# Performance work log

Hardware: AMD Instinct MI355X
Metric: run time of the kernel (lower is better)

## Reference

```python
import jax, jax.numpy as jnp
import numpy as np
import math

D, S, B = 64, 2048, 16  # head_dim, seq_len, batch (inputs stored as [D, S, B])


def setup_inputs() -> dict:
    key = jax.random.key(0)
    kq, kk, kv = jax.random.split(key, 3)
    return {
        "Q": jax.random.normal(kq, (D, S, B), dtype=jnp.float32),
        "K": jax.random.normal(kk, (D, S, B), dtype=jnp.float32),
        "V": jax.random.normal(kv, (D, S, B), dtype=jnp.float32),
        "d_k": S,
    }


def reference(Q, K, V, d_k):
    # transpose(0, 2): [D, S, B] -> [B, S, D]
    q = jnp.transpose(Q, (2, 1, 0))
    k = jnp.transpose(K, (2, 1, 0))
    v = jnp.transpose(V, (2, 1, 0))
    # bmm(_Q, K_T) * 1/sqrt(d_k): [B, S, S]
    scores = jnp.einsum("bsd,btd->bst", q, k) * (1.0 / math.sqrt(d_k))
    # original does view(-1, d_k) + Softmax over dim=1; with d_k == last dim
    # this is a softmax over the key axis. Dropout is identity in eval mode.
    probs = jax.nn.softmax(scores, axis=-1)
    out = jnp.einsum("bst,btd->bsd", probs, v)  # [B, S, D]
    # transpose(0, 2) back: [D, S, B]
    return jnp.transpose(out, (2, 1, 0))
```

## Files before the change

kernel.cpp:

```cpp
#include <hip/hip_runtime.h>

#define D_ 64
#define S_ 2048
#define B_ 16
#define QT 64
#define KVT 128

typedef short short8 __attribute__((ext_vector_type(8)));
typedef short short4a __attribute__((ext_vector_type(4)));
typedef float floatx4 __attribute__((ext_vector_type(4)));
typedef unsigned uint2v __attribute__((ext_vector_type(2)));

#define SC2 (1.4426950408889634f / 45.254833995939045f)

__device__ __forceinline__ unsigned short f2bf(float f) {
  unsigned u = __builtin_bit_cast(unsigned, f);
  u += 0x7fffu + ((u >> 16) & 1u);
  return (unsigned short)(u >> 16);
}

__device__ __forceinline__ floatx4 mfma16(short4a a, short4a b, floatx4 c) {
#if __has_builtin(__builtin_amdgcn_mfma_f32_16x16x16bf16_1k)
  return __builtin_amdgcn_mfma_f32_16x16x16bf16_1k(a, b, c, 0, 0, 0);
#else
  floatx4 d;
  asm volatile("v_mfma_f32_16x16x16_bf16 %0, %1, %2, %3"
               : "=v"(d) : "v"(a), "v"(b), "v"(c));
  return d;
#endif
}

__global__ __launch_bounds__(256) void pack_all(const float* __restrict__ Q,
                                                const float* __restrict__ K,
                                                const float* __restrict__ V,
                                                unsigned short* __restrict__ Qp,
                                                unsigned short* __restrict__ Kp,
                                                unsigned short* __restrict__ Vt) {
  __shared__ __align__(16) unsigned short tile[256][72];
  const int t = threadIdx.x;
  const int bid = blockIdx.x;
  if (bid < 256) {
    const bool isK = bid >= 128;
    const float* src = isK ? K : Q;
    unsigned short* dst = isK ? Kp : Qp;
    const float scale = isK ? SC2 : 1.0f;
    const int s0 = (bid & 127) * 16;
#pragma unroll
    for (int i = 0; i < 16; i++) {
      int j = i * 256 + t;
      int d = j >> 6;
      int sb4 = (j & 63) * 4;
      const float4 v = *(const float4*)(src + (size_t)d * (S_ * B_) + s0 * B_ + sb4);
      float vv[4] = {v.x, v.y, v.z, v.w};
#pragma unroll
      for (int k = 0; k < 4; k++) {
        int sb = sb4 + k;
        tile[(sb & 15) * 16 + (sb >> 4)][d] = f2bf(vv[k] * scale);
      }
    }
    __syncthreads();
#pragma unroll
    for (int i = 0; i < 8; i++) {
      int j = i * 256 + t;
      int r = j >> 3, c = j & 7;
      int b = r >> 4, si = r & 15;
      uint4 v = *(const uint4*)(&tile[r][c * 8]);
      *(uint4*)(dst + ((size_t)(b * S_ + s0 + si) * D_ + c * 8)) = v;
    }
  } else {
    const int vb = bid - 256;
    const int s0 = (vb & 31) * 64;
    const int d0 = (vb >> 5) * 16;
#pragma unroll
    for (int i = 0; i < 16; i++) {
      int j = i * 256 + t;
      int dd = j >> 8;
      int sb4 = (j & 255) * 4;
      const float4 v = *(const float4*)(V + (size_t)(d0 + dd) * (S_ * B_) + s0 * B_ + sb4);
      float vv[4] = {v.x, v.y, v.z, v.w};
#pragma unroll
      for (int k = 0; k < 4; k++) {
        int sb = sb4 + k;
        tile[(sb & 15) * 16 + dd][sb >> 4] = f2bf(vv[k]);
      }
    }
    __syncthreads();
#pragma unroll
    for (int i = 0; i < 8; i++) {
      int j = i * 256 + t;
      int r = j >> 3, c = j & 7;
      int b = r >> 4, dd = r & 15;
      uint4 v = *(const uint4*)(&tile[r][c * 8]);
      *(uint4*)(Vt + ((size_t)(b * D_ + d0 + dd) * S_ + s0 + c * 8)) = v;
    }
  }
}

__global__ __launch_bounds__(256, 2) void attn(const unsigned short* __restrict__ Qp,
                                               const unsigned short* __restrict__ Kp,
                                               const unsigned short* __restrict__ Vt,
                                               float* __restrict__ Ot) {
  __shared__ __align__(16) char smem_[69632 + 1024];
  float* red = (float*)smem_;
  float* lred = (float*)(smem_ + 69632);
  unsigned short* Vbuf0 = (unsigned short*)smem_;
  unsigned short* Vbuf1 = (unsigned short*)(smem_ + 17408);

  const int tid = threadIdx.x;
  const int w = tid >> 6, l = tid & 63, g = l >> 4, ln = l & 15;
  const int b = blockIdx.x & 15;
  const int q0 = (int)(blockIdx.x >> 4) * QT;
  const int kvw = w * 32;

  const unsigned short* Qb = Qp + (size_t)b * S_ * D_;
  const unsigned short* Kb = Kp + (size_t)b * S_ * D_;
  const unsigned short* Vb = Vt + (size_t)b * D_ * S_;

  short8 qf[4][2];
#pragma unroll
  for (int nf = 0; nf < 4; nf++)
#pragma unroll
    for (int ks = 0; ks < 2; ks++)
      qf[nf][ks] = *(const short8*)(Qb + (size_t)(q0 + nf * 16 + ln) * D_ + ks * 32 + g * 8);

  short8 kf[2][2];
#pragma unroll
  for (int mf = 0; mf < 2; mf++)
#pragma unroll
    for (int ks = 0; ks < 2; ks++)
      kf[mf][ks] = *(const short8*)(Kb + (size_t)(kvw + mf * 16 + ln) * D_ + ks * 32 + g * 8);

  {
    uint4 vstg[4];
#pragma unroll
    for (int i = 0; i < 4; i++) {
      int idx = i * 256 + tid, r = idx >> 4, c = idx & 15;
      vstg[i] = *(const uint4*)(Vb + (size_t)r * S_ + c * 8);
    }
#pragma unroll
    for (int i = 0; i < 4; i++) {
      int idx = i * 256 + tid, r = idx >> 4, c = idx & 15;
      *(uint4*)(&Vbuf0[r * 136 + c * 8]) = vstg[i];
    }
  }
  __syncthreads();

  const short4a ones = {(short)0x3F80, (short)0x3F80, (short)0x3F80, (short)0x3F80};
  floatx4 oacc[4][4];
  floatx4 dacc[4];
#pragma unroll
  for (int mfd = 0; mfd < 4; mfd++)
#pragma unroll
    for (int nf = 0; nf < 4; nf++) oacc[mfd][nf] = (floatx4){0.f, 0.f, 0.f, 0.f};
#pragma unroll
  for (int nf = 0; nf < 4; nf++) dacc[nf] = (floatx4){0.f, 0.f, 0.f, 0.f};

  for (int t = 0; t < 16; t++) {
    const int kvn = ((t + 1) * KVT) & (S_ - 1);

    uint4 vstg[4];
#pragma unroll
    for (int i = 0; i < 4; i++) {
      int idx = i * 256 + tid, r = idx >> 4, c = idx & 15;
      vstg[i] = *(const uint4*)(Vb + (size_t)r * S_ + kvn + c * 8);
    }

    floatx4 sacc[2][4];
#pragma unroll
    for (int mf = 0; mf < 2; mf++)
#pragma unroll
      for (int nf = 0; nf < 4; nf++) sacc[mf][nf] = (floatx4){0.f, 0.f, 0.f, 0.f};
#pragma unroll
    for (int ks = 0; ks < 2; ks++)
#pragma unroll
      for (int mf = 0; mf < 2; mf++)
#pragma unroll
        for (int nf = 0; nf < 4; nf++)
          sacc[mf][nf] = __builtin_amdgcn_mfma_f32_16x16x32_bf16(kf[mf][ks], qf[nf][ks],
                                                                 sacc[mf][nf], 0, 0, 0);

#pragma unroll
    for (int mf = 0; mf < 2; mf++)
#pragma unroll
      for (int ks = 0; ks < 2; ks++)
        kf[mf][ks] = *(const short8*)(Kb + (size_t)(kvn + kvw + mf * 16 + ln) * D_ + ks * 32 + g * 8);

    short4a pb[2][4];
#pragma unroll
    for (int mf = 0; mf < 2; mf++)
#pragma unroll
      for (int nf = 0; nf < 4; nf++) {
        unsigned u0 = __builtin_bit_cast(unsigned, __builtin_amdgcn_exp2f(sacc[mf][nf][0])) + 0x8000u;
        unsigned u1 = __builtin_bit_cast(unsigned, __builtin_amdgcn_exp2f(sacc[mf][nf][1])) + 0x8000u;
        unsigned u2 = __builtin_bit_cast(unsigned, __builtin_amdgcn_exp2f(sacc[mf][nf][2])) + 0x8000u;
        unsigned u3 = __builtin_bit_cast(unsigned, __builtin_amdgcn_exp2f(sacc[mf][nf][3])) + 0x8000u;
        unsigned lo = __builtin_amdgcn_perm(u1, u0, 0x07060302u);
        unsigned hi = __builtin_amdgcn_perm(u3, u2, 0x07060302u);
        pb[mf][nf] = __builtin_bit_cast(short4a, (uint2v){lo, hi});
      }

#pragma unroll
    for (int mf = 0; mf < 2; mf++)
#pragma unroll
      for (int nf = 0; nf < 4; nf++)
        dacc[nf] = mfma16(ones, pb[mf][nf], dacc[nf]);

    unsigned short* vw = ((t + 1) & 1) ? Vbuf1 : Vbuf0;
#pragma unroll
    for (int i = 0; i < 4; i++) {
      int idx = i * 256 + tid, r = idx >> 4, c = idx & 15;
      *(uint4*)(&vw[r * 136 + c * 8]) = vstg[i];
    }

    const unsigned short* vr = (t & 1) ? Vbuf1 : Vbuf0;
#pragma unroll
    for (int mfd = 0; mfd < 4; mfd++)
#pragma unroll
      for (int mf = 0; mf < 2; mf++) {
        short4a vf = *(const short4a*)(&vr[(mfd * 16 + ln) * 136 + kvw + mf * 16 + g * 4]);
#pragma unroll
        for (int nf = 0; nf < 4; nf++)
          oacc[mfd][nf] = mfma16(vf, pb[mf][nf], oacc[mfd][nf]);
      }
    __syncthreads();
  }

  if (g == 0) {
#pragma unroll
    for (int nf = 0; nf < 4; nf++) lred[w * 64 + nf * 16 + ln] = dacc[nf][0];
  }
#pragma unroll
  for (int mfd = 0; mfd < 4; mfd++)
#pragma unroll
    for (int nf = 0; nf < 4; nf++)
      *(floatx4*)(&red[w * 4352 + (nf * 16 + ln) * 68 + mfd * 16 + g * 4]) = oacc[mfd][nf];
  __syncthreads();

  const int q = l;
  const float denom = lred[q] + lred[64 + q] + lred[128 + q] + lred[192 + q];
  const float linv = 1.0f / denom;
#pragma unroll
  for (int i = 0; i < 4; i++) {
    floatx4 s = (floatx4){0.f, 0.f, 0.f, 0.f};
#pragma unroll
    for (int w2 = 0; w2 < 4; w2++)
      s += *(const floatx4*)(&red[w2 * 4352 + q * 68 + w * 16 + i * 4]);
    s *= linv;
#pragma unroll
    for (int r = 0; r < 4; r++)
      Ot[(size_t)(b * D_ + w * 16 + i * 4 + r) * S_ + q0 + q] = s[r];
  }
}

__global__ __launch_bounds__(256) void unpack_o(const float* __restrict__ Ot,
                                                float* __restrict__ out) {
  const int d0 = (int)(blockIdx.x & 7) * 8;
  const int s0 = (int)(blockIdx.x >> 3) * 64;
  __shared__ float u[8 * 1024];
  const int t = threadIdx.x;
#pragma unroll
  for (int i = 0; i < 8; i++) {
    int j = i * 256 + t;
    int d = j >> 8, bb = (j >> 4) & 15, c = j & 15;
    float4 v = *(const float4*)(Ot + (size_t)(bb * D_ + d0 + d) * S_ + s0 + c * 4);
    float vv[4] = {v.x, v.y, v.z, v.w};
#pragma unroll
    for (int k = 0; k < 4; k++) {
      int si = c * 4 + k;
      int W = si * 16 + bb;
      int Wp = W ^ ((si & 15) << 2);
      u[d * 1024 + Wp] = vv[k];
    }
  }
  __syncthreads();
#pragma unroll
  for (int i = 0; i < 8; i++) {
    int j = i * 256 + t;
    int d = j >> 8, c2 = j & 255;
    int G = c2 ^ ((c2 >> 2) & 15);
    float4 v = *(const float4*)(&u[d * 1024 + G * 4]);
    *(float4*)(out + (size_t)(d0 + d) * (S_ * B_) + s0 * B_ + c2 * 4) = v;
  }
}

extern "C" void kernel_launch(void* const* d_in, const int* in_sizes, int n_in,
                              void* d_out, int out_size, void* d_ws, size_t ws_size,
                              hipStream_t stream) {
  const float* Q = (const float*)d_in[0];
  const float* K = (const float*)d_in[1];
  const float* V = (const float*)d_in[2];
  float* out = (float*)d_out;
  char* ws = (char*)d_ws;
  unsigned short* Qp = (unsigned short*)(ws);
  unsigned short* Kp = (unsigned short*)(ws + (4u << 20));
  unsigned short* Vt = (unsigned short*)(ws + (8u << 20));
  float* Ot = (float*)(ws + (12u << 20));

  hipLaunchKernelGGL(pack_all, dim3(384), dim3(256), 0, stream, Q, K, V, Qp, Kp, Vt);
  hipLaunchKernelGGL(attn, dim3(512), dim3(256), 0, stream, Qp, Kp, Vt, Ot);
  hipLaunchKernelGGL(unpack_o, dim3(256), dim3(256), 0, stream, Ot, out);
}
```

Measured before the change: 110.8 us.

## Load V fragments directly to registers and drop LDS staging and per-tile syncs

The attention loop no longer stages V tiles through double-buffered shared memory with a barrier per tile. Each wave now loads its own V fragments straight from global memory into registers, double-buffered in a manually unrolled two-step loop. The row-sum denominator is accumulated in fp32 with adds and cross-lane shuffles instead of extra MFMAs against a ones vector. The pack kernel's shared tile gets XOR swizzling to cut bank conflicts. In exchange, each wave issues narrow 8-byte strided global loads for V and uses more registers.

```diff
diff --git a/kernel.cpp b/kernel.cpp
--- a/kernel.cpp
+++ b/kernel.cpp
@@ -20,14 +20,7 @@
 }
 
 __device__ __forceinline__ floatx4 mfma16(short4a a, short4a b, floatx4 c) {
-#if __has_builtin(__builtin_amdgcn_mfma_f32_16x16x16bf16_1k)
   return __builtin_amdgcn_mfma_f32_16x16x16bf16_1k(a, b, c, 0, 0, 0);
-#else
-  floatx4 d;
-  asm volatile("v_mfma_f32_16x16x16_bf16 %0, %1, %2, %3"
-               : "=v"(d) : "v"(a), "v"(b), "v"(c));
-  return d;
-#endif
 }
 
 __global__ __launch_bounds__(256) void pack_all(const float* __restrict__ Q,
@@ -55,7 +48,9 @@
 #pragma unroll
       for (int k = 0; k < 4; k++) {
         int sb = sb4 + k;
-        tile[(sb & 15) * 16 + (sb >> 4)][d] = f2bf(vv[k] * scale);
+        int row = (sb & 15) * 16 + (sb >> 4);
+        int sw = (((row >> 3) & 1) << 3) | (((row >> 6) & 3) << 4);
+        tile[row][d ^ sw] = f2bf(vv[k] * scale);
       }
     }
     __syncthreads();
@@ -64,7 +59,8 @@
       int j = i * 256 + t;
       int r = j >> 3, c = j & 7;
       int b = r >> 4, si = r & 15;
-      uint4 v = *(const uint4*)(&tile[r][c * 8]);
+      int sw = (((r >> 3) & 1) << 3) | (((r >> 6) & 3) << 4);
+      uint4 v = *(const uint4*)(&tile[r][(c * 8) ^ sw]);
       *(uint4*)(dst + ((size_t)(b * S_ + s0 + si) * D_ + c * 8)) = v;
     }
   } else {
@@ -81,7 +77,9 @@
 #pragma unroll
       for (int k = 0; k < 4; k++) {
         int sb = sb4 + k;
-        tile[(sb & 15) * 16 + dd][sb >> 4] = f2bf(vv[k]);
+        int row = (sb & 15) * 16 + dd;
+        int sw = ((row >> 6) & 3) << 3;
+        tile[row][(sb >> 4) ^ sw] = f2bf(vv[k]);
       }
     }
     __syncthreads();
@@ -90,7 +88,8 @@
       int j = i * 256 + t;
       int r = j >> 3, c = j & 7;
       int b = r >> 4, dd = r & 15;
-      uint4 v = *(const uint4*)(&tile[r][c * 8]);
+      int sw = ((r >> 6) & 3) << 3;
+      uint4 v = *(const uint4*)(&tile[r][(c * 8) ^ sw]);
       *(uint4*)(Vt + ((size_t)(b * D_ + d0 + dd) * S_ + s0 + c * 8)) = v;
     }
   }
@@ -100,11 +99,8 @@
                                                const unsigned short* __restrict__ Kp,
                                                const unsigned short* __restrict__ Vt,
                                                float* __restrict__ Ot) {
-  __shared__ __align__(16) char smem_[69632 + 1024];
-  float* red = (float*)smem_;
-  float* lred = (float*)(smem_ + 69632);
-  unsigned short* Vbuf0 = (unsigned short*)smem_;
-  unsigned short* Vbuf1 = (unsigned short*)(smem_ + 17408);
+  __shared__ __align__(16) float red[4 * 64 * 68];
+  __shared__ float lred[4 * 64];
 
   const int tid = threadIdx.x;
   const int w = tid >> 6, l = tid & 63, g = l >> 4, ln = l & 15;
@@ -123,47 +119,38 @@
     for (int ks = 0; ks < 2; ks++)
       qf[nf][ks] = *(const short8*)(Qb + (size_t)(q0 + nf * 16 + ln) * D_ + ks * 32 + g * 8);
 
-  short8 kf[2][2];
+  floatx4 oacc[4][4];
+#pragma unroll
+  for (int mfd = 0; mfd < 4; mfd++)
+#pragma unroll
+    for (int nf = 0; nf < 4; nf++) oacc[mfd][nf] = (floatx4){0.f, 0.f, 0.f, 0.f};
+  float lpart[4] = {0.f, 0.f, 0.f, 0.f};
+
+  short8 kfA[2][2], kfB[2][2];
+  short4a vfA[4][2], vfB[4][2];
 #pragma unroll
   for (int mf = 0; mf < 2; mf++)
 #pragma unroll
     for (int ks = 0; ks < 2; ks++)
-      kf[mf][ks] = *(const short8*)(Kb + (size_t)(kvw + mf * 16 + ln) * D_ + ks * 32 + g * 8);
-
-  {
-    uint4 vstg[4];
-#pragma unroll
-    for (int i = 0; i < 4; i++) {
-      int idx = i * 256 + tid, r = idx >> 4, c = idx & 15;
-      vstg[i] = *(const uint4*)(Vb + (size_t)r * S_ + c * 8);
-    }
-#pragma unroll
-    for (int i = 0; i < 4; i++) {
-      int idx = i * 256 + tid, r = idx >> 4, c = idx & 15;
-      *(uint4*)(&Vbuf0[r * 136 + c * 8]) = vstg[i];
-    }
-  }
-  __syncthreads();
-
-  const short4a ones = {(short)0x3F80, (short)0x3F80, (short)0x3F80, (short)0x3F80};
-  floatx4 oacc[4][4];
-  floatx4 dacc[4];
+      kfA[mf][ks] = *(const short8*)(Kb + (size_t)(kvw + mf * 16 + ln) * D_ + ks * 32 + g * 8);
 #pragma unroll
   for (int mfd = 0; mfd < 4; mfd++)
 #pragma unroll
-    for (int nf = 0; nf < 4; nf++) oacc[mfd][nf] = (floatx4){0.f, 0.f, 0.f, 0.f};
-#pragma unroll
-  for (int nf = 0; nf < 4; nf++) dacc[nf] = (floatx4){0.f, 0.f, 0.f, 0.f};
-
-  for (int t = 0; t < 16; t++) {
-    const int kvn = ((t + 1) * KVT) & (S_ - 1);
-
-    uint4 vstg[4];
-#pragma unroll
-    for (int i = 0; i < 4; i++) {
-      int idx = i * 256 + tid, r = idx >> 4, c = idx & 15;
-      vstg[i] = *(const uint4*)(Vb + (size_t)r * S_ + kvn + c * 8);
-    }
+    for (int mf = 0; mf < 2; mf++)
+      vfA[mfd][mf] = *(const short4a*)(Vb + (size_t)(mfd * 16 + ln) * S_ + kvw + mf * 16 + g * 4);
+
+  auto tile_step = [&](short8 (&kfc)[2][2], short8 (&kfn)[2][2],
+                       short4a (&vfc)[4][2], short4a (&vfn)[4][2], int kvn) {
+#pragma unroll
+    for (int mf = 0; mf < 2; mf++)
+#pragma unroll
+      for (int ks = 0; ks < 2; ks++)
+        kfn[mf][ks] = *(const short8*)(Kb + (size_t)(kvn + kvw + mf * 16 + ln) * D_ + ks * 32 + g * 8);
+#pragma unroll
+    for (int mfd = 0; mfd < 4; mfd++)
+#pragma unroll
+      for (int mf = 0; mf < 2; mf++)
+        vfn[mfd][mf] = *(const short4a*)(Vb + (size_t)(mfd * 16 + ln) * S_ + kvn + kvw + mf * 16 + g * 4);
 
     floatx4 sacc[2][4];
 #pragma unroll
@@ -176,58 +163,53 @@
       for (int mf = 0; mf < 2; mf++)
 #pragma unroll
         for (int nf = 0; nf < 4; nf++)
-          sacc[mf][nf] = __builtin_amdgcn_mfma_f32_16x16x32_bf16(kf[mf][ks], qf[nf][ks],
+          sacc[mf][nf] = __builtin_amdgcn_mfma_f32_16x16x32_bf16(kfc[mf][ks], qf[nf][ks],
                                                                  sacc[mf][nf], 0, 0, 0);
 
-#pragma unroll
-    for (int mf = 0; mf < 2; mf++)
-#pragma unroll
-      for (int ks = 0; ks < 2; ks++)
-        kf[mf][ks] = *(const short8*)(Kb + (size_t)(kvn + kvw + mf * 16 + ln) * D_ + ks * 32 + g * 8);
-
     short4a pb[2][4];
 #pragma unroll
     for (int mf = 0; mf < 2; mf++)
 #pragma unroll
       for (int nf = 0; nf < 4; nf++) {
-        unsigned u0 = __builtin_bit_cast(unsigned, __builtin_amdgcn_exp2f(sacc[mf][nf][0])) + 0x8000u;
-        unsigned u1 = __builtin_bit_cast(unsigned, __builtin_amdgcn_exp2f(sacc[mf][nf][1])) + 0x8000u;
-        unsigned u2 = __builtin_bit_cast(unsigned, __builtin_amdgcn_exp2f(sacc[mf][nf][2])) + 0x8000u;
-        unsigned u3 = __builtin_bit_cast(unsigned, __builtin_amdgcn_exp2f(sacc[mf][nf][3])) + 0x8000u;
+        float p0 = __builtin_amdgcn_exp2f(sacc[mf][nf][0]);
+        float p1 = __builtin_amdgcn_exp2f(sacc[mf][nf][1]);
+        float p2 = __builtin_amdgcn_exp2f(sacc[mf][nf][2]);
+        float p3 = __builtin_amdgcn_exp2f(sacc[mf][nf][3]);
+        lpart[nf] += (p0 + p1) + (p2 + p3);
+        unsigned u0 = __builtin_bit_cast(unsigned, p0) + 0x8000u;
+        unsigned u1 = __builtin_bit_cast(unsigned, p1) + 0x8000u;
+        unsigned u2 = __builtin_bit_cast(unsigned, p2) + 0x8000u;
+        unsigned u3 = __builtin_bit_cast(unsigned, p3) + 0x8000u;
         unsigned lo = __builtin_amdgcn_perm(u1, u0, 0x07060302u);
         unsigned hi = __builtin_amdgcn_perm(u3, u2, 0x07060302u);
         pb[mf][nf] = __builtin_bit_cast(short4a, (uint2v){lo, hi});
       }
 
 #pragma unroll
-    for (int mf = 0; mf < 2; mf++)
-#pragma unroll
-      for (int nf = 0; nf < 4; nf++)
-        dacc[nf] = mfma16(ones, pb[mf][nf], dacc[nf]);
-
-    unsigned short* vw = ((t + 1) & 1) ? Vbuf1 : Vbuf0;
-#pragma unroll
-    for (int i = 0; i < 4; i++) {
-      int idx = i * 256 + tid, r = idx >> 4, c = idx & 15;
-      *(uint4*)(&vw[r * 136 + c * 8]) = vstg[i];
-    }
-
-    const unsigned short* vr = (t & 1) ? Vbuf1 : Vbuf0;
-#pragma unroll
     for (int mfd = 0; mfd < 4; mfd++)
 #pragma unroll
-      for (int mf = 0; mf < 2; mf++) {
-        short4a vf = *(const short4a*)(&vr[(mfd * 16 + ln) * 136 + kvw + mf * 16 + g * 4]);
+      for (int mf = 0; mf < 2; mf++)
 #pragma unroll
         for (int nf = 0; nf < 4; nf++)
-          oacc[mfd][nf] = mfma16(vf, pb[mf][nf], oacc[mfd][nf]);
-      }
-    __syncthreads();
-  }
-
+          oacc[mfd][nf] = mfma16(vfc[mfd][mf], pb[mf][nf], oacc[mfd][nf]);
+  };
+
+  for (int it = 0; it < 8; it++) {
+    tile_step(kfA, kfB, vfA, vfB, (it * 2 + 1) * KVT);
+    tile_step(kfB, kfA, vfB, vfA, ((it * 2 + 2) * KVT) & (S_ - 1));
+  }
+
+  float lsum[4];
+#pragma unroll
+  for (int nf = 0; nf < 4; nf++) {
+    float v = lpart[nf];
+    v += __shfl_xor(v, 16);
+    v += __shfl_xor(v, 32);
+    lsum[nf] = v;
+  }
   if (g == 0) {
 #pragma unroll
-    for (int nf = 0; nf < 4; nf++) lred[w * 64 + nf * 16 + ln] = dacc[nf][0];
+    for (int nf = 0; nf < 4; nf++) lred[w * 64 + nf * 16 + ln] = lsum[nf];
   }
 #pragma unroll
   for (int mfd = 0; mfd < 4; mfd++)
```

Result: slower. 128.8 us (+16.3%).
